# Kernel optimization log

Hardware: AMD Instinct MI355X
Metric: run time of the kernel (lower is better)

## Reference

```python
import jax, jax.numpy as jnp
import numpy as np

TEMP = 0.07  # InfoCNECauchy temperature


def setup_inputs() -> dict:
    key = jax.random.key(0)
    k1, k2 = jax.random.split(key)
    features = jax.random.normal(k1, (8192, 512), dtype=jnp.float32)  # 2N x d, two augmented views
    labels = jax.random.randint(k2, (8192,), 0, 100)  # unused in selfsupervised mode
    return {"features": features, "labels": labels}


def reference(features, labels):
    n2 = features.shape[0]
    n = n2 // 2
    # squared pairwise Euclidean distances (== torch.cdist(...)**2)
    sq = jnp.sum(features * features, axis=1)
    d2 = jnp.maximum(sq[:, None] + sq[None, :] - 2.0 * (features @ features.T), 0.0)
    # Cauchy similarity kernel: 1 / ((dist / t)^2 + 1)
    sim = 1.0 / (d2 / (TEMP * TEMP) + 1.0)
    # selfsupervised mask: row i is positive only with its partner view i^N,
    # so the masked mean-log reduces to log(sim[i, partner(i)])
    idx = jnp.arange(n2)
    partner = jnp.where(idx < n, idx + n, idx - n)
    pos = jnp.mean(jnp.log(sim[idx, partner]))
    # negatives: sum over row excluding the diagonal (sim diag == 1)
    neg = jnp.mean(jnp.log(jnp.sum(sim, axis=1) - jnp.diagonal(sim)))
    return -(pos - neg)
```

## Files before the change

### kernel.cpp

```cpp
#include <hip/hip_runtime.h>


#define N2 8192
#define DIM 512
#define NT 64
#define NTILES (NT * (NT + 1) / 2)
#define T2 0.0049f

typedef float floatx4 __attribute__((ext_vector_type(4)));
typedef __bf16 bf16x8 __attribute__((ext_vector_type(8)));
typedef __bf16 bf16x4 __attribute__((ext_vector_type(4)));

__device__ __forceinline__ void load_to_lds16(const void* g, void* l) {
  auto gp = (const __attribute__((address_space(1))) void*)(reinterpret_cast<uintptr_t>(g));
  auto lp = (__attribute__((address_space(3))) void*)(reinterpret_cast<uintptr_t>(l));
  __builtin_amdgcn_global_load_lds(gp, lp, 16, 0, 0);
}

__global__ __launch_bounds__(256) void prep_kernel(const float* __restrict__ f,
                                                   __bf16* __restrict__ fbf,
                                                   float* __restrict__ sq,
                                                   float* __restrict__ rowsum) {
  const int t = threadIdx.x;
  if (t < 2) rowsum[blockIdx.x * 2 + t] = 0.f;
  const int row = blockIdx.x * 2 + (t >> 7);
  const int ci = (t & 127) * 4;
  const float4 v = *(const float4*)(f + (size_t)row * DIM + ci);
  bf16x4 b;
  b[0] = (__bf16)v.x; b[1] = (__bf16)v.y; b[2] = (__bf16)v.z; b[3] = (__bf16)v.w;
  *(bf16x4*)(fbf + (size_t)row * DIM + ci) = b;
  float s = v.x * v.x + v.y * v.y + v.z * v.z + v.w * v.w;
#pragma unroll
  for (int off = 1; off < 64; off <<= 1) s += __shfl_xor(s, off, 64);
  __shared__ float red[4];
  if ((t & 63) == 0) red[t >> 6] = s;
  __syncthreads();
  if ((t & 127) == 0) sq[row] = red[t >> 6] + red[(t >> 6) + 1];
}

__global__ __launch_bounds__(256) void gemm_kernel(const __bf16* __restrict__ fbf,
                                                   const float* __restrict__ sq,
                                                   float* __restrict__ rowsum,
                                                   float* __restrict__ spart) {
  __shared__ __bf16 aT[128 * 64];
  __shared__ __bf16 bT[128 * 64];

  int by, bx;
  {
    const int x = blockIdx.x & 7;
    int kk = blockIdx.x >> 3;
    int band = x;
    const int n1 = 250 - 16 * x;
    if (kk >= n1) { kk -= n1; band = 15 - x; }
    const int by0 = band * 4;
    int bxx = by0;
    int cnt;
    while (kk >= (cnt = min(4, bxx - by0 + 1))) { kk -= cnt; ++bxx; }
    by = by0 + kk;
    bx = bxx;
  }
  const int brow = by * 128;
  const int bcol = bx * 128;
  const bool diag = (by == bx);

  const int t = threadIdx.x;
  const int lane = t & 63;
  const int w = t >> 6;
  const int wrow = (w >> 1) * 64;
  const int wcol = (w & 1) * 64;
  const int q4 = lane >> 4;
  const int lc = lane & 15;

  floatx4 acc[4][4] = {};

  int grow[2], gofs[2];
#pragma unroll
  for (int it = 0; it < 2; ++it) {
    const int slot = it * 256 + t;
    const int rp = slot >> 3;
    const int u = (slot & 7) ^ (rp & 7);
    grow[it] = rp * 2 + (u >> 2);
    gofs[it] = (u & 3) * 8;
  }

  const int up = (((lc & 1) * 4) + q4) ^ (lc >> 1);
  const int rhalf = lc >> 1;

  for (int kt = 0; kt < DIM / 64; ++kt) {
    const int k0 = kt * 64;
#pragma unroll
    for (int it = 0; it < 2; ++it) {
#pragma unroll
      for (int ks = 0; ks < 2; ++ks) {
        load_to_lds16(fbf + (size_t)(brow + grow[it]) * DIM + k0 + ks * 32 + gofs[it],
                      &aT[ks * 4096 + it * 2048 + t * 8]);
        load_to_lds16(fbf + (size_t)(bcol + grow[it]) * DIM + k0 + ks * 32 + gofs[it],
                      &bT[ks * 4096 + it * 2048 + t * 8]);
      }
    }
    __syncthreads();
#pragma unroll
    for (int ks = 0; ks < 2; ++ks) {
      bf16x8 af[4], bfr[4];
#pragma unroll
      for (int mr = 0; mr < 4; ++mr)
        af[mr] = *(const bf16x8*)&aT[ks * 4096 + ((wrow >> 1) + mr * 8 + rhalf) * 64 + up * 8];
#pragma unroll
      for (int mc = 0; mc < 4; ++mc)
        bfr[mc] = *(const bf16x8*)&bT[ks * 4096 + ((wcol >> 1) + mc * 8 + rhalf) * 64 + up * 8];
#pragma unroll
      for (int mr = 0; mr < 4; ++mr)
#pragma unroll
        for (int mc = 0; mc < 4; ++mc)
          acc[mr][mc] =
              __builtin_amdgcn_mfma_f32_16x16x32_bf16(af[mr], bfr[mc], acc[mr][mc], 0, 0, 0);
    }
    __syncthreads();
  }

  float sqc[4];
#pragma unroll
  for (int mc = 0; mc < 4; ++mc) sqc[mc] = sq[bcol + wcol + mc * 16 + lc];

  float cs[4] = {0.f, 0.f, 0.f, 0.f};

#pragma unroll
  for (int mr = 0; mr < 4; ++mr) {
#pragma unroll
    for (int reg = 0; reg < 4; ++reg) {
      const int r = brow + wrow + mr * 16 + q4 * 4 + reg;
      const float sr = sq[r];
      const int pc = r ^ (N2 / 2);
      float rs = 0.f;
#pragma unroll
      for (int mc = 0; mc < 4; ++mc) {
        const int c = bcol + wcol + mc * 16 + lc;
        const float g = acc[mr][mc][reg];
        const float d2 = fmaxf(sr + sqc[mc] - 2.f * g, 0.f);
        const float s = T2 * __builtin_amdgcn_rcpf(d2 + T2);
        if (c != r) rs += s;
        cs[mc] += s;
        if (c == pc) { spart[r] = s; spart[pc] = s; }
      }
#pragma unroll
      for (int off = 1; off < 16; off <<= 1) rs += __shfl_xor(rs, off, 64);
      if (lc == 0) atomicAdd(&rowsum[r], rs);
    }
  }

  if (!diag) {
#pragma unroll
    for (int mc = 0; mc < 4; ++mc) {
      float v = cs[mc];
      v += __shfl_xor(v, 16, 64);
      v += __shfl_xor(v, 32, 64);
      if (lane < 16) atomicAdd(&rowsum[bcol + wcol + mc * 16 + lane], v);
    }
  }
}

__global__ __launch_bounds__(256) void final_kernel(const float* __restrict__ rowsum,
                                                    const float* __restrict__ spart,
                                                    float* __restrict__ out) {
  const int t = threadIdx.x;
  float a = 0.f;
  for (int r = t; r < N2; r += 256) a += logf(rowsum[r]) - logf(spart[r]);
#pragma unroll
  for (int off = 1; off < 64; off <<= 1) a += __shfl_xor(a, off, 64);
  __shared__ float red[4];
  if ((t & 63) == 0) red[t >> 6] = a;
  __syncthreads();
  if (t == 0) out[0] = (red[0] + red[1] + red[2] + red[3]) * (1.0f / (float)N2);
}

extern "C" void kernel_launch(void* const* d_in, const int* in_sizes, int n_in,
                              void* d_out, int out_size, void* d_ws, size_t ws_size,
                              hipStream_t stream) {
  const float* features = (const float*)d_in[0];
  float* out = (float*)d_out;

  char* ws = (char*)d_ws;
  __bf16* fbf = (__bf16*)ws;
  float* sq = (float*)(ws + (size_t)N2 * DIM * sizeof(__bf16));
  float* rowsum = sq + N2;
  float* spart = rowsum + N2;

  prep_kernel<<<N2 / 2, 256, 0, stream>>>(features, fbf, sq, rowsum);
  gemm_kernel<<<NTILES, 256, 0, stream>>>(fbf, sq, rowsum, spart);
  final_kernel<<<1, 256, 0, stream>>>(rowsum, spart, out);
}
```

Before: 141.7 us.

## Load MFMA operands directly from global memory, dropping LDS staging

The GEMM kernel stops staging A/B tiles through shared memory with global_load_lds and barriers. Each wave now loads its bf16x8 fragments straight from global memory (relying on L1/L2 for reuse between waves) and runs a 32-wide K loop unrolled by 4. It also adds an occupancy hint of 4 blocks per CU to __launch_bounds__. This removes LDS traffic and __syncthreads, but each A/B row is now fetched by two waves, and the per-lane 16-byte loads with a DIM stride are poorly coalesced.

```diff
diff --git a/kernel.cpp b/kernel.cpp
--- a/kernel.cpp
+++ b/kernel.cpp
@@ -10,12 +10,6 @@
 typedef float floatx4 __attribute__((ext_vector_type(4)));
 typedef __bf16 bf16x8 __attribute__((ext_vector_type(8)));
 typedef __bf16 bf16x4 __attribute__((ext_vector_type(4)));
-
-__device__ __forceinline__ void load_to_lds16(const void* g, void* l) {
-  auto gp = (const __attribute__((address_space(1))) void*)(reinterpret_cast<uintptr_t>(g));
-  auto lp = (__attribute__((address_space(3))) void*)(reinterpret_cast<uintptr_t>(l));
-  __builtin_amdgcn_global_load_lds(gp, lp, 16, 0, 0);
-}
 
 __global__ __launch_bounds__(256) void prep_kernel(const float* __restrict__ f,
                                                    __bf16* __restrict__ fbf,
@@ -38,13 +32,10 @@
   if ((t & 127) == 0) sq[row] = red[t >> 6] + red[(t >> 6) + 1];
 }
 
-__global__ __launch_bounds__(256) void gemm_kernel(const __bf16* __restrict__ fbf,
-                                                   const float* __restrict__ sq,
-                                                   float* __restrict__ rowsum,
-                                                   float* __restrict__ spart) {
-  __shared__ __bf16 aT[128 * 64];
-  __shared__ __bf16 bT[128 * 64];
-
+__global__ __launch_bounds__(256, 4) void gemm_kernel(const __bf16* __restrict__ fbf,
+                                                      const float* __restrict__ sq,
+                                                      float* __restrict__ rowsum,
+                                                      float* __restrict__ spart) {
   int by, bx;
   {
     const int x = blockIdx.x & 7;
@@ -73,49 +64,24 @@
 
   floatx4 acc[4][4] = {};
 
-  int grow[2], gofs[2];
+  const __bf16* pa = fbf + (size_t)(brow + wrow + lc) * DIM + q4 * 8;
+  const __bf16* pb = fbf + (size_t)(bcol + wcol + lc) * DIM + q4 * 8;
+
+#pragma unroll 4
+  for (int kt = 0; kt < DIM / 32; ++kt) {
+    const int k0 = kt * 32;
+    bf16x8 af[4], bfr[4];
 #pragma unroll
-  for (int it = 0; it < 2; ++it) {
-    const int slot = it * 256 + t;
-    const int rp = slot >> 3;
-    const int u = (slot & 7) ^ (rp & 7);
-    grow[it] = rp * 2 + (u >> 2);
-    gofs[it] = (u & 3) * 8;
-  }
-
-  const int up = (((lc & 1) * 4) + q4) ^ (lc >> 1);
-  const int rhalf = lc >> 1;
-
-  for (int kt = 0; kt < DIM / 64; ++kt) {
-    const int k0 = kt * 64;
+    for (int m = 0; m < 4; ++m) {
+      af[m] = *(const bf16x8*)(pa + (size_t)m * 16 * DIM + k0);
+      bfr[m] = *(const bf16x8*)(pb + (size_t)m * 16 * DIM + k0);
+    }
 #pragma unroll
-    for (int it = 0; it < 2; ++it) {
-#pragma unroll
-      for (int ks = 0; ks < 2; ++ks) {
-        load_to_lds16(fbf + (size_t)(brow + grow[it]) * DIM + k0 + ks * 32 + gofs[it],
-                      &aT[ks * 4096 + it * 2048 + t * 8]);
-        load_to_lds16(fbf + (size_t)(bcol + grow[it]) * DIM + k0 + ks * 32 + gofs[it],
-                      &bT[ks * 4096 + it * 2048 + t * 8]);
-      }
-    }
-    __syncthreads();
-#pragma unroll
-    for (int ks = 0; ks < 2; ++ks) {
-      bf16x8 af[4], bfr[4];
-#pragma unroll
-      for (int mr = 0; mr < 4; ++mr)
-        af[mr] = *(const bf16x8*)&aT[ks * 4096 + ((wrow >> 1) + mr * 8 + rhalf) * 64 + up * 8];
+    for (int mr = 0; mr < 4; ++mr)
 #pragma unroll
       for (int mc = 0; mc < 4; ++mc)
-        bfr[mc] = *(const bf16x8*)&bT[ks * 4096 + ((wcol >> 1) + mc * 8 + rhalf) * 64 + up * 8];
-#pragma unroll
-      for (int mr = 0; mr < 4; ++mr)
-#pragma unroll
-        for (int mc = 0; mc < 4; ++mc)
-          acc[mr][mc] =
-              __builtin_amdgcn_mfma_f32_16x16x32_bf16(af[mr], bfr[mc], acc[mr][mc], 0, 0, 0);
-    }
-    __syncthreads();
+        acc[mr][mc] =
+            __builtin_amdgcn_mfma_f32_16x16x32_bf16(af[mr], bfr[mc], acc[mr][mc], 0, 0, 0);
   }
 
   float sqc[4];
```

Result: slower. 232.4 us (+64.1%).

## Double-buffer LDS tiles to prefetch next K-slice during MFMA compute

Applied to the files above, without the earlier changes.

Splits the A/B shared-memory tiles into two buffers and issues the async global-to-LDS loads for the next K-step before computing on the current one. This replaces the old load, barrier, compute, barrier sequence with a prologue load and one barrier per iteration. The goal is to hide global load latency behind the MFMA work. The cost is doubled LDS use per block (64 KB), which may cut the number of resident blocks per CU.

```diff
diff --git a/kernel.cpp b/kernel.cpp
--- a/kernel.cpp
+++ b/kernel.cpp
@@ -42,8 +42,8 @@
                                                    const float* __restrict__ sq,
                                                    float* __restrict__ rowsum,
                                                    float* __restrict__ spart) {
-  __shared__ __bf16 aT[128 * 64];
-  __shared__ __bf16 bT[128 * 64];
+  __shared__ __bf16 aT[2][2][4096];
+  __shared__ __bf16 bT[2][2][4096];
 
   int by, bx;
   {
@@ -86,28 +86,33 @@
   const int up = (((lc & 1) * 4) + q4) ^ (lc >> 1);
   const int rhalf = lc >> 1;
 
+#define STAGE(kt, d) do {                                                     \
+    const int k0_ = (kt) * 64;                                                \
+    _Pragma("unroll") for (int it = 0; it < 2; ++it) {                        \
+      _Pragma("unroll") for (int ks = 0; ks < 2; ++ks) {                      \
+        load_to_lds16(fbf + (size_t)(brow + grow[it]) * DIM + k0_ + ks * 32 + gofs[it], \
+                      &aT[d][ks][it * 2048 + t * 8]);                         \
+        load_to_lds16(fbf + (size_t)(bcol + grow[it]) * DIM + k0_ + ks * 32 + gofs[it], \
+                      &bT[d][ks][it * 2048 + t * 8]);                         \
+      }                                                                       \
+    }                                                                         \
+  } while (0)
+
+  STAGE(0, 0);
+  __syncthreads();
+
   for (int kt = 0; kt < DIM / 64; ++kt) {
-    const int k0 = kt * 64;
-#pragma unroll
-    for (int it = 0; it < 2; ++it) {
-#pragma unroll
-      for (int ks = 0; ks < 2; ++ks) {
-        load_to_lds16(fbf + (size_t)(brow + grow[it]) * DIM + k0 + ks * 32 + gofs[it],
-                      &aT[ks * 4096 + it * 2048 + t * 8]);
-        load_to_lds16(fbf + (size_t)(bcol + grow[it]) * DIM + k0 + ks * 32 + gofs[it],
-                      &bT[ks * 4096 + it * 2048 + t * 8]);
-      }
-    }
-    __syncthreads();
+    const int d = kt & 1;
+    if (kt + 1 < DIM / 64) STAGE(kt + 1, d ^ 1);
 #pragma unroll
     for (int ks = 0; ks < 2; ++ks) {
       bf16x8 af[4], bfr[4];
 #pragma unroll
       for (int mr = 0; mr < 4; ++mr)
-        af[mr] = *(const bf16x8*)&aT[ks * 4096 + ((wrow >> 1) + mr * 8 + rhalf) * 64 + up * 8];
+        af[mr] = *(const bf16x8*)&aT[d][ks][((wrow >> 1) + mr * 8 + rhalf) * 64 + up * 8];
 #pragma unroll
       for (int mc = 0; mc < 4; ++mc)
-        bfr[mc] = *(const bf16x8*)&bT[ks * 4096 + ((wcol >> 1) + mc * 8 + rhalf) * 64 + up * 8];
+        bfr[mc] = *(const bf16x8*)&bT[d][ks][((wcol >> 1) + mc * 8 + rhalf) * 64 + up * 8];
 #pragma unroll
       for (int mr = 0; mr < 4; ++mr)
 #pragma unroll
```

Result: slower. 151.2 us (+6.7%).
